# Optimization experiments

Hardware: AMD Instinct MI355X
Metric: run time of the kernel (lower is better)

The kernel has to match this reference:

```python
import jax, jax.numpy as jnp
import numpy as np

H, C = 4, 32          # num_heads, hidden_channels
NEG_ATT = 0.2         # GAT attention leaky_relu slope (PyG default)
NEG_ACT = 0.01        # F.leaky_relu default slope applied after each conv


def gat_conv(x_src, x_dst, Wsrc, Wdst, a_src, a_dst, bias, src_idx, dst_idx, n_dst):
    """One bipartite GATConv (add_self_loops=False, concat=True)."""
    hs = (x_src @ Wsrc).reshape(-1, H, C)            # [Ns,H,C]
    hd = (x_dst @ Wdst).reshape(-1, H, C)            # [Nd,H,C]
    a_s = (hs * a_src).sum(-1)                       # [Ns,H]
    a_d = (hd * a_dst).sum(-1)                       # [Nd,H]
    e = jax.nn.leaky_relu(a_s[src_idx] + a_d[dst_idx], NEG_ATT)  # [E,H]
    m = jax.ops.segment_max(e, dst_idx, num_segments=n_dst)      # [Nd,H]
    ex = jnp.exp(e - m[dst_idx])
    denom = jax.ops.segment_sum(ex, dst_idx, num_segments=n_dst)
    alpha = ex / (denom[dst_idx] + 1e-16)            # edge softmax over dst
    msg = hs[src_idx] * alpha[:, :, None]            # [E,H,C]
    out = jax.ops.segment_sum(msg, dst_idx, num_segments=n_dst)  # [Nd,H,C]
    return out.reshape(n_dst, H * C) + bias


def setup_inputs() -> dict:
    key = jax.random.key(0)
    ks = jax.random.split(key, 40)
    it = iter(range(40))
    Nu, Nm, E, D, O = 100000, 20000, 500000, 64, 64
    HC = H * C

    def rn(shape, s=0.1):
        return jax.random.normal(ks[next(it)], shape, jnp.float32) * s

    def ri(n, hi):
        return jax.random.randint(ks[next(it)], (n,), 0, hi)

    return {
        "user_ids": jnp.arange(Nu), "movie_ids": jnp.arange(Nm),
        "um_src": ri(E, Nu), "um_dst": ri(E, Nm),
        "mu_src": ri(E, Nm), "mu_dst": ri(E, Nu),
        "user_emb": rn((Nu, D)), "movie_emb": rn((Nm, D)),
        "l1_um_Wsrc": rn((D, HC)), "l1_um_Wdst": rn((D, HC)),
        "l1_um_asrc": rn((H, C)), "l1_um_adst": rn((H, C)), "l1_um_b": rn((HC,)),
        "l1_mu_Wsrc": rn((D, HC)), "l1_mu_Wdst": rn((D, HC)),
        "l1_mu_asrc": rn((H, C)), "l1_mu_adst": rn((H, C)), "l1_mu_b": rn((HC,)),
        "l2_um_W": rn((HC, HC)), "l2_um_asrc": rn((H, C)), "l2_um_adst": rn((H, C)), "l2_um_b": rn((HC,)),
        "l2_mu_W": rn((HC, HC)), "l2_mu_asrc": rn((H, C)), "l2_mu_adst": rn((H, C)), "l2_mu_b": rn((HC,)),
        "Wo": rn((HC, O)), "bo": rn((O,)),
    }


def reference(user_ids, movie_ids, um_src, um_dst, mu_src, mu_dst,
              user_emb, movie_emb,
              l1_um_Wsrc, l1_um_Wdst, l1_um_asrc, l1_um_adst, l1_um_b,
              l1_mu_Wsrc, l1_mu_Wdst, l1_mu_asrc, l1_mu_adst, l1_mu_b,
              l2_um_W, l2_um_asrc, l2_um_adst, l2_um_b,
              l2_mu_W, l2_mu_asrc, l2_mu_adst, l2_mu_b,
              Wo, bo):
    xu = user_emb[user_ids]
    xm = movie_emb[movie_ids]
    Nu, Nm = xu.shape[0], xm.shape[0]
    # layer 1 (HeteroConv sum: each dst type receives exactly one edge type here)
    hm = gat_conv(xu, xm, l1_um_Wsrc, l1_um_Wdst, l1_um_asrc, l1_um_adst, l1_um_b, um_src, um_dst, Nm)
    hu = gat_conv(xm, xu, l1_mu_Wsrc, l1_mu_Wdst, l1_mu_asrc, l1_mu_adst, l1_mu_b, mu_src, mu_dst, Nu)
    xu = jax.nn.leaky_relu(hu, NEG_ACT)
    xm = jax.nn.leaky_relu(hm, NEG_ACT)
    # layer 2 (non-bipartite in_channels int => shared lin for src and dst)
    hm = gat_conv(xu, xm, l2_um_W, l2_um_W, l2_um_asrc, l2_um_adst, l2_um_b, um_src, um_dst, Nm)
    hu = gat_conv(xm, xu, l2_mu_W, l2_mu_W, l2_mu_asrc, l2_mu_adst, l2_mu_b, mu_src, mu_dst, Nu)
    xu = jax.nn.leaky_relu(hu, NEG_ACT)
    xm = jax.nn.leaky_relu(hm, NEG_ACT)
    out_user = xu @ Wo + bo
    out_movie = xm @ Wo + bo
    return out_user, out_movie, xu, xm
```

## Files before the change

### kernel.cpp

```cpp
#include <hip/hip_runtime.h>
#include <hip/hip_bf16.h>
#include <cstdint>


#define HC 128
#define HH 4
#define WPART 256
#define EPB 2048

typedef __attribute__((ext_vector_type(8))) short bf16x8;
typedef __attribute__((ext_vector_type(4))) float f32x4;

__device__ __forceinline__ short f2bf(float f) {
    return __builtin_bit_cast(short, __float2bfloat16(f));
}
__device__ __forceinline__ float bf2f(ushort u) {
    return __builtin_bit_cast(float, ((unsigned)u) << 16);
}

struct VT { const float* W[8]; const float* a[8]; float* v[8]; };
__global__ void make_v_all_k(VT t) {
    int gid = blockIdx.x * 256 + threadIdx.x;
    int task, base;
    if (gid < 1024) { task = gid >> 8; base = gid & 255; }
    else if (gid < 3072) { int g = gid - 1024; task = 4 + (g >> 9); base = g & 511; }
    else return;
    int k = base >> 2, h = base & 3;
    int coff = (task & 1) * 4;
    const float* wr = t.W[task] + (size_t)k * HC + h * 32;
    const float* ar = t.a[task] + h * 32;
    float s = 0.f;
    #pragma unroll
    for (int c = 0; c < 32; ++c) s = fmaf(wr[c], ar[c], s);
    t.v[task][k * 8 + coff + h] = s;
}

struct PT { const float* W[5]; const float* V[5]; ushort* Wb[5];
            int K[5]; int Nw[5]; int start[6]; };
__global__ void pack_all_k(PT t) {
    int gid = blockIdx.x * 256 + threadIdx.x;
    if (gid >= t.start[5]) return;
    int task = 0;
    while (gid >= t.start[task + 1]) ++task;
    int loc = gid - t.start[task];
    int K = t.K[task], Nw = t.Nw[task];
    int n = loc / K, k = loc % K;
    float v = 0.f;
    if (n < Nw) v = t.W[task][(size_t)k * Nw + n];
    else if (t.V[task] != nullptr && n < Nw + 8) v = t.V[task][k * 8 + (n - Nw)];
    t.Wb[task][loc] = (ushort)f2bf(v);
}

template <int NT, int MODE, bool ABF>
__global__ __launch_bounds__(256) void gemm_dual_k(
    const void* A0, const int* idx0, const ushort* Wb0, ushort* hsb0,
    ushort* atts0, float* attd0, float* C0, const float* bias0, int M0, int nb0,
    const void* A1, const int* idx1, const ushort* Wb1, ushort* hsb1,
    ushort* atts1, float* attd1, float* C1, const float* bias1, int M1,
    int K, int ldc) {
    const void* A; const int* aidx; const ushort* Wb; ushort* hsb;
    ushort* atts; float* attd; float* C; const float* bias; int M, bid;
    if ((int)blockIdx.x < nb0) {
        A = A0; aidx = idx0; Wb = Wb0; hsb = hsb0; atts = atts0; attd = attd0;
        C = C0; bias = bias0; M = M0; bid = blockIdx.x;
    } else {
        A = A1; aidx = idx1; Wb = Wb1; hsb = hsb1; atts = atts1; attd = attd1;
        C = C1; bias = bias1; M = M1; bid = blockIdx.x - nb0;
    }
    int lane = threadIdx.x & 63;
    int wave = threadIdx.x >> 6;
    int m_base = bid * 128 + wave * 32;
    int lm = lane & 15;
    int kg = lane >> 4;

    int r0 = m_base + lm, r1 = r0 + 16;
    int cr0 = r0 < M ? r0 : M - 1;
    int cr1 = r1 < M ? r1 : M - 1;
    int row0 = aidx ? aidx[cr0] : cr0;
    int row1 = aidx ? aidx[cr1] : cr1;
    const ushort* bp = Wb + (size_t)lm * K + kg * 8;

    f32x4 acc[2][NT] = {};
    for (int k0 = 0; k0 < K; k0 += 32) {
        bf16x8 a[2];
        if (ABF) {
            const ushort* a0p = (const ushort*)A + (size_t)row0 * K + kg * 8;
            const ushort* a1p = (const ushort*)A + (size_t)row1 * K + kg * 8;
            a[0] = *reinterpret_cast<const bf16x8*>(a0p + k0);
            a[1] = *reinterpret_cast<const bf16x8*>(a1p + k0);
        } else {
            const float* a0p = (const float*)A + (size_t)row0 * K + kg * 8;
            const float* a1p = (const float*)A + (size_t)row1 * K + kg * 8;
            float af[2][8];
            *reinterpret_cast<float4*>(&af[0][0]) = *reinterpret_cast<const float4*>(a0p + k0);
            *reinterpret_cast<float4*>(&af[0][4]) = *reinterpret_cast<const float4*>(a0p + k0 + 4);
            *reinterpret_cast<float4*>(&af[1][0]) = *reinterpret_cast<const float4*>(a1p + k0);
            *reinterpret_cast<float4*>(&af[1][4]) = *reinterpret_cast<const float4*>(a1p + k0 + 4);
            #pragma unroll
            for (int mi = 0; mi < 2; ++mi)
                #pragma unroll
                for (int j = 0; j < 8; ++j) a[mi][j] = f2bf(af[mi][j]);
        }
        #pragma unroll
        for (int nt = 0; nt < NT; ++nt) {
            bf16x8 b = *reinterpret_cast<const bf16x8*>(bp + (size_t)nt * 16 * K + k0);
            acc[0][nt] = __builtin_amdgcn_mfma_f32_16x16x32_bf16(a[0], b, acc[0][nt], 0, 0, 0);
            acc[1][nt] = __builtin_amdgcn_mfma_f32_16x16x32_bf16(a[1], b, acc[1][nt], 0, 0, 0);
        }
    }
    #pragma unroll
    for (int mi = 0; mi < 2; ++mi) {
        int rowb = m_base + mi * 16 + kg * 4;
        if (MODE == 0) {
            #pragma unroll
            for (int nt = 0; nt < NT - 1; ++nt) {
                int col = nt * 16 + lm;
                #pragma unroll
                for (int r = 0; r < 4; ++r) {
                    int row = rowb + r;
                    if (row < M) hsb[(size_t)row * HC + col] = (ushort)f2bf(acc[mi][nt][r]);
                }
            }
            #pragma unroll
            for (int r = 0; r < 4; ++r) {
                int row = rowb + r;
                if (row < M) {
                    float v = acc[mi][NT - 1][r];
                    if (lm < 4) atts[(size_t)row * 4 + lm] = (ushort)f2bf(v);
                    else if (lm < 8) attd[(size_t)row * 4 + (lm - 4)] = v;
                }
            }
        } else {
            #pragma unroll
            for (int nt = 0; nt < NT; ++nt) {
                int col = nt * 16 + lm;
                float bv = bias[col];
                #pragma unroll
                for (int r = 0; r < 4; ++r) {
                    int row = rowb + r;
                    if (row < M) C[(size_t)row * ldc + col] = acc[mi][nt][r] + bv;
                }
            }
        }
    }
}

__global__ __launch_bounds__(256) void part_count_k(
    const int* __restrict__ d0, int E0,
    const int* __restrict__ d1, int E1, int Nm,
    int* __restrict__ cntmat, int NB1) {
    __shared__ int lh[WPART];
    int t = threadIdx.x;
    lh[t] = 0;
    __syncthreads();
    int base = blockIdx.x * EPB + t;
    #pragma unroll
    for (int j = 0; j < EPB / 256; ++j) {
        int e = base + j * 256;
        int key = -1;
        if (e < E0) key = d0[e];
        else if (e - E0 < E1) key = Nm + d1[e - E0];
        if (key >= 0) atomicAdd(&lh[key >> 9], 1);
    }
    __syncthreads();
    cntmat[(size_t)t * NB1 + blockIdx.x] = lh[t];
}

__global__ __launch_bounds__(256) void part_scatter_k(
    const int* __restrict__ s0, const int* __restrict__ d0, int E0,
    const int* __restrict__ s1, const int* __restrict__ d1, int E1, int Nm,
    const int* __restrict__ scanned, int NB1, int2* __restrict__ buf) {
    __shared__ int lb[WPART];
    __shared__ int lc[WPART];
    int t = threadIdx.x;
    lb[t] = scanned[(size_t)t * NB1 + blockIdx.x];
    lc[t] = 0;
    __syncthreads();
    int base = blockIdx.x * EPB + t;
    #pragma unroll
    for (int j = 0; j < EPB / 256; ++j) {
        int e = base + j * 256;
        int key = -1, src = 0;
        if (e < E0) { key = d0[e]; src = s0[e]; }
        else if (e - E0 < E1) { key = Nm + d1[e - E0]; src = s1[e - E0]; }
        if (key >= 0) {
            int w = key >> 9;
            int r = atomicAdd(&lc[w], 1);
            buf[lb[w] + r] = make_int2(src, key);
        }
    }
}

__global__ __launch_bounds__(512) void csort_k(
    const int2* __restrict__ buf, const int* __restrict__ scanned, int NB1,
    int E, int NK, int* __restrict__ rs, int* __restrict__ csr) {
    __shared__ int c1[512];
    __shared__ int ls[512];
    int b = blockIdx.x;
    int t = threadIdx.x;
    int lo = scanned[(size_t)b * NB1];
    int hi = (b + 1 < WPART) ? scanned[(size_t)(b + 1) * NB1] : E;
    int keylo = b << 9;
    c1[t] = 0;
    __syncthreads();
    for (int i = lo + t; i < hi; i += 512)
        atomicAdd(&c1[buf[i].y - keylo], 1);
    __syncthreads();
    int v = c1[t];
    ls[t] = v;
    __syncthreads();
    for (int off = 1; off < 512; off <<= 1) {
        int x = (t >= off) ? ls[t - off] : 0;
        __syncthreads();
        ls[t] += x;
        __syncthreads();
    }
    ls[t] -= v;
    int gk = keylo + t;
    if (gk <= NK) rs[gk] = lo + ls[t];
    c1[t] = 0;
    __syncthreads();
    for (int i = lo + t; i < hi; i += 512) {
        int2 p = buf[i];
        int k = p.y - keylo;
        int r = atomicAdd(&c1[k], 1);
        csr[lo + ls[k] + r] = p.x;
    }
}

__global__ void scan_block_k(const int* __restrict__ deg, int n,
                             int* __restrict__ out, int* __restrict__ partial) {
    __shared__ int s[256];
    int i = blockIdx.x * 256 + threadIdx.x;
    int v = (i < n) ? deg[i] : 0;
    s[threadIdx.x] = v;
    __syncthreads();
    for (int off = 1; off < 256; off <<= 1) {
        int x = (threadIdx.x >= off) ? s[threadIdx.x - off] : 0;
        __syncthreads();
        s[threadIdx.x] += x;
        __syncthreads();
    }
    if (i < n) out[i] = s[threadIdx.x] - v;
    if (threadIdx.x == 255) partial[blockIdx.x] = s[255];
}

__global__ void scan_partial_k(int* __restrict__ partial, int nb) {
    __shared__ int s[512];
    int t = threadIdx.x;
    int v = (t < nb) ? partial[t] : 0;
    s[t] = v;
    __syncthreads();
    for (int off = 1; off < 512; off <<= 1) {
        int x = (t >= off) ? s[t - off] : 0;
        __syncthreads();
        s[t] += x;
        __syncthreads();
    }
    if (t < nb) partial[t] = s[t] - v;
}

__global__ void add_off_k(int* __restrict__ out, const int* __restrict__ partial, int n) {
    int i = blockIdx.x * 256 + threadIdx.x;
    if (i < n) out[i] += partial[blockIdx.x];
}

template <bool WF32, bool WBF>
__global__ __launch_bounds__(256) void agg16_dual_k(
    const int* __restrict__ rs0, const int* __restrict__ csr0,
    const ushort* __restrict__ hsb0, const ushort* __restrict__ atts0,
    const float* __restrict__ attd0, const float* __restrict__ bias0,
    float* __restrict__ out0, ushort* __restrict__ outb0, int n0,
    const int* __restrict__ rs1, const int* __restrict__ csr1,
    const ushort* __restrict__ hsb1, const ushort* __restrict__ atts1,
    const float* __restrict__ attd1, const float* __restrict__ bias1,
    float* __restrict__ out1, ushort* __restrict__ outb1, int n1) {
    int g = (int)((blockIdx.x * 256u + threadIdx.x) >> 4);
    const int* rs; const int* csr; const ushort* hsb; const ushort* atts;
    const float* attd; const float* bias; float* out; ushort* outb; int node;
    if (g < n0) {
        rs = rs0; csr = csr0; hsb = hsb0; atts = atts0; attd = attd0;
        bias = bias0; out = out0; outb = outb0; node = g;
    } else {
        node = g - n0;
        if (node >= n1) return;
        rs = rs1; csr = csr1; hsb = hsb1; atts = atts1; attd = attd1;
        bias = bias1; out = out1; outb = outb1;
    }
    int c = threadIdx.x & 15;
    int h = c >> 2;
    float ad = attd[node * 4 + h];
    int s0 = rs[node], s1 = rs[node + 1];
    float acc[8] = {};
    float wsum = 0.f;
    int i = s0;
    for (; i + 4 <= s1; i += 4) {
        int sx[4];
        #pragma unroll
        for (int j = 0; j < 4; ++j) sx[j] = csr[i + j];
        bf16x8 hv[4]; float el[4];
        #pragma unroll
        for (int j = 0; j < 4; ++j) {
            hv[j] = *reinterpret_cast<const bf16x8*>(hsb + (size_t)sx[j] * HC + 8 * c);
            el[j] = bf2f(atts[(size_t)sx[j] * 4 + h]);
        }
        #pragma unroll
        for (int j = 0; j < 4; ++j) {
            float e = el[j] + ad;
            e = e > 0.f ? e : 0.2f * e;
            float w = __expf(e);
            wsum += w;
            #pragma unroll
            for (int k = 0; k < 8; ++k)
                acc[k] = fmaf(w, bf2f((ushort)hv[j][k]), acc[k]);
        }
    }
    for (; i < s1; ++i) {
        int src = csr[i];
        bf16x8 hv = *reinterpret_cast<const bf16x8*>(hsb + (size_t)src * HC + 8 * c);
        float e = bf2f(atts[(size_t)src * 4 + h]) + ad;
        e = e > 0.f ? e : 0.2f * e;
        float w = __expf(e);
        wsum += w;
        #pragma unroll
        for (int k = 0; k < 8; ++k)
            acc[k] = fmaf(w, bf2f((ushort)hv[k]), acc[k]);
    }
    float inv = 1.f / (wsum + 1e-16f);
    float v[8];
    #pragma unroll
    for (int k = 0; k < 8; ++k) {
        v[k] = fmaf(acc[k], inv, bias[8 * c + k]);
        v[k] = v[k] > 0.f ? v[k] : 0.01f * v[k];
    }
    if (WF32) {
        float4 o0 = make_float4(v[0], v[1], v[2], v[3]);
        float4 o1 = make_float4(v[4], v[5], v[6], v[7]);
        reinterpret_cast<float4*>(out + (size_t)node * HC + 8 * c)[0] = o0;
        reinterpret_cast<float4*>(out + (size_t)node * HC + 8 * c)[1] = o1;
    }
    if (WBF) {
        bf16x8 u;
        #pragma unroll
        for (int k = 0; k < 8; ++k) u[k] = f2bf(v[k]);
        *reinterpret_cast<bf16x8*>(outb + (size_t)node * HC + 8 * c) = u;
    }
}

extern "C" void kernel_launch(void* const* d_in, const int* in_sizes, int n_in,
                              void* d_out, int out_size, void* d_ws, size_t ws_size,
                              hipStream_t stream) {
    const int Nu = in_sizes[0];
    const int Nm = in_sizes[1];
    const int E1 = in_sizes[2];
    const int E2 = in_sizes[4];
    const int D  = in_sizes[6] / Nu;
    const int O  = in_sizes[27];
    const int E  = E1 + E2;
    const int NK = Nm + Nu;

    const int*   user_ids  = (const int*)d_in[0];
    const int*   movie_ids = (const int*)d_in[1];
    const int*   um_src    = (const int*)d_in[2];
    const int*   um_dst    = (const int*)d_in[3];
    const int*   mu_src    = (const int*)d_in[4];
    const int*   mu_dst    = (const int*)d_in[5];
    const float* user_emb  = (const float*)d_in[6];
    const float* movie_emb = (const float*)d_in[7];
    const float* l1_um_Wsrc = (const float*)d_in[8];
    const float* l1_um_Wdst = (const float*)d_in[9];
    const float* l1_um_asrc = (const float*)d_in[10];
    const float* l1_um_adst = (const float*)d_in[11];
    const float* l1_um_b    = (const float*)d_in[12];
    const float* l1_mu_Wsrc = (const float*)d_in[13];
    const float* l1_mu_Wdst = (const float*)d_in[14];
    const float* l1_mu_asrc = (const float*)d_in[15];
    const float* l1_mu_adst = (const float*)d_in[16];
    const float* l1_mu_b    = (const float*)d_in[17];
    const float* l2_um_W    = (const float*)d_in[18];
    const float* l2_um_asrc = (const float*)d_in[19];
    const float* l2_um_adst = (const float*)d_in[20];
    const float* l2_um_b    = (const float*)d_in[21];
    const float* l2_mu_W    = (const float*)d_in[22];
    const float* l2_mu_asrc = (const float*)d_in[23];
    const float* l2_mu_adst = (const float*)d_in[24];
    const float* l2_mu_b    = (const float*)d_in[25];
    const float* Wo         = (const float*)d_in[26];
    const float* bo         = (const float*)d_in[27];

    auto cdiv = [](int a, int b) { return (a + b - 1) / b; };
    const int NB1 = cdiv(E, EPB);
    const int CM  = WPART * NB1;

    char* p = (char*)d_ws;
    auto alloc = [&](size_t bytes) { void* r = p; p += (bytes + 255) & ~(size_t)255; return r; };
    ushort* hs_u = (ushort*)alloc((size_t)Nu * HC * 2);
    ushort* hs_m = (ushort*)alloc((size_t)Nm * HC * 2);
    ushort* XUb  = (ushort*)alloc((size_t)Nu * HC * 2);
    ushort* XMb  = (ushort*)alloc((size_t)Nm * HC * 2);
    ushort* atts_u = (ushort*)alloc((size_t)Nu * 4 * 2);
    ushort* atts_m = (ushort*)alloc((size_t)Nm * 4 * 2);
    float* attd_u = (float*)alloc((size_t)Nu * 4 * 4);
    float* attd_m = (float*)alloc((size_t)Nm * 4 * 4);
    float* V_u1  = (float*)alloc((size_t)HC * 8 * 4);
    float* V_m1  = (float*)alloc((size_t)HC * 8 * 4);
    float* V_u2  = (float*)alloc((size_t)HC * 8 * 4);
    float* V_m2  = (float*)alloc((size_t)HC * 8 * 4);
    ushort* Wb_u1 = (ushort*)alloc((size_t)144 * D * 2);
    ushort* Wb_m1 = (ushort*)alloc((size_t)144 * D * 2);
    ushort* Wb_u2 = (ushort*)alloc((size_t)144 * HC * 2);
    ushort* Wb_m2 = (ushort*)alloc((size_t)144 * HC * 2);
    ushort* Wb_o  = (ushort*)alloc((size_t)64 * HC * 2);
    int* rs      = (int*)alloc((size_t)(NK + 2) * 4);
    int* cntmat  = (int*)alloc((size_t)(CM + 256) * 4);
    int* scanned = (int*)alloc((size_t)(CM + 256) * 4);
    int2* buf    = (int2*)alloc((size_t)E * 8);
    int* csr     = (int*)alloc((size_t)E * 4);
    int* part    = (int*)alloc(1024 * 4);

    {
        VT vt;
        const float* Ws[8] = {l1_um_Wsrc, l1_mu_Wdst, l1_mu_Wsrc, l1_um_Wdst,
                              l2_um_W, l2_mu_W, l2_mu_W, l2_um_W};
        const float* as[8] = {l1_um_asrc, l1_mu_adst, l1_mu_asrc, l1_um_adst,
                              l2_um_asrc, l2_mu_adst, l2_mu_asrc, l2_um_adst};
        float* vs[8] = {V_u1, V_u1, V_m1, V_m1, V_u2, V_u2, V_m2, V_m2};
        for (int i = 0; i < 8; ++i) { vt.W[i] = Ws[i]; vt.a[i] = as[i]; vt.v[i] = vs[i]; }
        make_v_all_k<<<12, 256, 0, stream>>>(vt);

        PT pt;
        const float* pW[5] = {l1_um_Wsrc, l1_mu_Wsrc, l2_um_W, l2_mu_W, Wo};
        const float* pV[5] = {V_u1, V_m1, V_u2, V_m2, nullptr};
        ushort* pB[5] = {Wb_u1, Wb_m1, Wb_u2, Wb_m2, Wb_o};
        int pK[5] = {D, D, HC, HC, HC};
        int pN[5] = {HC, HC, HC, HC, 64};
        int cum = 0;
        for (int i = 0; i < 5; ++i) {
            pt.W[i] = pW[i]; pt.V[i] = pV[i]; pt.Wb[i] = pB[i];
            pt.K[i] = pK[i]; pt.Nw[i] = pN[i];
            pt.start[i] = cum;
            cum += (i < 4 ? 144 : 64) * pK[i];
        }
        pt.start[5] = cum;
        pack_all_k<<<cdiv(cum, 256), 256, 0, stream>>>(pt);
    }

    part_count_k<<<NB1, 256, 0, stream>>>(um_dst, E1, mu_dst, E2, Nm, cntmat, NB1);
    {
        int nb = cdiv(CM, 256);
        scan_block_k<<<nb, 256, 0, stream>>>(cntmat, CM, scanned, part);
        scan_partial_k<<<1, 512, 0, stream>>>(part, nb);
        add_off_k<<<nb, 256, 0, stream>>>(scanned, part, CM);
    }
    part_scatter_k<<<NB1, 256, 0, stream>>>(um_src, um_dst, E1, mu_src, mu_dst, E2,
                                            Nm, scanned, NB1, buf);
    csort_k<<<WPART, 512, 0, stream>>>(buf, scanned, NB1, E, NK, rs, csr);

    float* OU = (float*)d_out;
    float* OM = OU + (size_t)Nu * O;
    float* XU = OM + (size_t)Nm * O;
    float* XM = XU + (size_t)Nu * HC;

    int gbU = cdiv(Nu, 128), gbM = cdiv(Nm, 128);
    int aggBlocks = cdiv((Nm + Nu) * 16, 256);

    gemm_dual_k<9, 0, false><<<gbU + gbM, 256, 0, stream>>>(
        user_emb, user_ids, Wb_u1, hs_u, atts_u, attd_u, nullptr, nullptr, Nu, gbU,
        movie_emb, movie_ids, Wb_m1, hs_m, atts_m, attd_m, nullptr, nullptr, Nm,
        D, 0);
    agg16_dual_k<false, true><<<aggBlocks, 256, 0, stream>>>(
        rs, csr, hs_u, atts_u, attd_m, l1_um_b, nullptr, XMb, Nm,
        rs + Nm, csr, hs_m, atts_m, attd_u, l1_mu_b, nullptr, XUb, Nu);

    gemm_dual_k<9, 0, true><<<gbU + gbM, 256, 0, stream>>>(
        XUb, nullptr, Wb_u2, hs_u, atts_u, attd_u, nullptr, nullptr, Nu, gbU,
        XMb, nullptr, Wb_m2, hs_m, atts_m, attd_m, nullptr, nullptr, Nm,
        HC, 0);
    agg16_dual_k<true, false><<<aggBlocks, 256, 0, stream>>>(
        rs, csr, hs_u, atts_u, attd_m, l2_um_b, XM, nullptr, Nm,
        rs + Nm, csr, hs_m, atts_m, attd_u, l2_mu_b, XU, nullptr, Nu);

    gemm_dual_k<4, 1, false><<<gbU + gbM, 256, 0, stream>>>(
        XU, nullptr, Wb_o, nullptr, nullptr, nullptr, OU, bo, Nu, gbU,
        XM, nullptr, Wb_o, nullptr, nullptr, nullptr, OM, bo, Nm,
        HC, O);
}
```

Baseline: 213.6 us.

## Fuse output projection into layer-2 aggregation kernel via MFMA epilogue

The final Wo projection GEMM is folded into the layer-2 aggregation kernel. Each block stages its 16 aggregated node rows as bf16 in shared memory and runs a 16x16x32 bf16 MFMA against Wo to write the output rows directly. This removes one kernel launch and the re-read of the fp32 XU/XM activations. In exchange it adds a block-wide barrier and shared-memory traffic to the aggregation kernel, and the projection now uses bf16-rounded activations.

```diff
diff --git a/kernel.cpp b/kernel.cpp
--- a/kernel.cpp
+++ b/kernel.cpp
@@ -265,7 +265,7 @@
     if (i < n) out[i] += partial[blockIdx.x];
 }
 
-template <bool WF32, bool WBF>
+template <bool WF32, bool WBF, bool PROJ>
 __global__ __launch_bounds__(256) void agg16_dual_k(
     const int* __restrict__ rs0, const int* __restrict__ csr0,
     const ushort* __restrict__ hsb0, const ushort* __restrict__ atts0,
@@ -274,23 +274,28 @@
     const int* __restrict__ rs1, const int* __restrict__ csr1,
     const ushort* __restrict__ hsb1, const ushort* __restrict__ atts1,
     const float* __restrict__ attd1, const float* __restrict__ bias1,
-    float* __restrict__ out1, ushort* __restrict__ outb1, int n1) {
+    float* __restrict__ out1, ushort* __restrict__ outb1, int n1,
+    const ushort* __restrict__ Wbo, const float* __restrict__ bo,
+    float* __restrict__ pj0, float* __restrict__ pj1) {
     int g = (int)((blockIdx.x * 256u + threadIdx.x) >> 4);
+    int gl = (threadIdx.x >> 4) & 15;
     const int* rs; const int* csr; const ushort* hsb; const ushort* atts;
-    const float* attd; const float* bias; float* out; ushort* outb; int node;
+    const float* attd; const float* bias; float* out; ushort* outb;
+    int node; bool active = true;
     if (g < n0) {
         rs = rs0; csr = csr0; hsb = hsb0; atts = atts0; attd = attd0;
         bias = bias0; out = out0; outb = outb0; node = g;
     } else {
         node = g - n0;
-        if (node >= n1) return;
+        if (node >= n1) { active = false; node = 0; }
         rs = rs1; csr = csr1; hsb = hsb1; atts = atts1; attd = attd1;
         bias = bias1; out = out1; outb = outb1;
     }
     int c = threadIdx.x & 15;
     int h = c >> 2;
     float ad = attd[node * 4 + h];
-    int s0 = rs[node], s1 = rs[node + 1];
+    int s0 = 0, s1 = 0;
+    if (active) { s0 = rs[node]; s1 = rs[node + 1]; }
     float acc[8] = {};
     float wsum = 0.f;
     int i = s0;
@@ -333,17 +338,47 @@
         v[k] = fmaf(acc[k], inv, bias[8 * c + k]);
         v[k] = v[k] > 0.f ? v[k] : 0.01f * v[k];
     }
-    if (WF32) {
+    if (active && WF32) {
         float4 o0 = make_float4(v[0], v[1], v[2], v[3]);
         float4 o1 = make_float4(v[4], v[5], v[6], v[7]);
         reinterpret_cast<float4*>(out + (size_t)node * HC + 8 * c)[0] = o0;
         reinterpret_cast<float4*>(out + (size_t)node * HC + 8 * c)[1] = o1;
     }
-    if (WBF) {
+    if (active && WBF) {
         bf16x8 u;
         #pragma unroll
         for (int k = 0; k < 8; ++k) u[k] = f2bf(v[k]);
         *reinterpret_cast<bf16x8*>(outb + (size_t)node * HC + 8 * c) = u;
+    }
+    if constexpr (PROJ) {
+        __shared__ ushort As[16][136];
+        bf16x8 u;
+        #pragma unroll
+        for (int k = 0; k < 8; ++k) u[k] = active ? f2bf(v[k]) : (short)0;
+        *reinterpret_cast<bf16x8*>(&As[gl][8 * c]) = u;
+        __syncthreads();
+        int lane = threadIdx.x & 63;
+        int wv = threadIdx.x >> 6;
+        int lm = lane & 15;
+        int kg = lane >> 4;
+        int col = wv * 16 + lm;
+        const ushort* bp = Wbo + (size_t)col * HC + kg * 8;
+        f32x4 pacc = {};
+        #pragma unroll
+        for (int k0 = 0; k0 < HC; k0 += 32) {
+            bf16x8 a = *reinterpret_cast<const bf16x8*>(&As[lm][k0 + kg * 8]);
+            bf16x8 b = *reinterpret_cast<const bf16x8*>(bp + k0);
+            pacc = __builtin_amdgcn_mfma_f32_16x16x32_bf16(a, b, pacc, 0, 0, 0);
+        }
+        float bv = bo[col];
+        int blockBase = blockIdx.x * 16;
+        #pragma unroll
+        for (int r = 0; r < 4; ++r) {
+            int slot = kg * 4 + r;
+            int ng = blockBase + slot;
+            if (ng < n0) pj0[(size_t)ng * 64 + col] = pacc[r] + bv;
+            else if (ng - n0 < n1) pj1[(size_t)(ng - n0) * 64 + col] = pacc[r] + bv;
+        }
     }
 }
 
@@ -468,20 +503,17 @@
         user_emb, user_ids, Wb_u1, hs_u, atts_u, attd_u, nullptr, nullptr, Nu, gbU,
         movie_emb, movie_ids, Wb_m1, hs_m, atts_m, attd_m, nullptr, nullptr, Nm,
         D, 0);
-    agg16_dual_k<false, true><<<aggBlocks, 256, 0, stream>>>(
+    agg16_dual_k<false, true, false><<<aggBlocks, 256, 0, stream>>>(
         rs, csr, hs_u, atts_u, attd_m, l1_um_b, nullptr, XMb, Nm,
-        rs + Nm, csr, hs_m, atts_m, attd_u, l1_mu_b, nullptr, XUb, Nu);
+        rs + Nm, csr, hs_m, atts_m, attd_u, l1_mu_b, nullptr, XUb, Nu,
+        nullptr, nullptr, nullptr, nullptr);
 
     gemm_dual_k<9, 0, true><<<gbU + gbM, 256, 0, stream>>>(
         XUb, nullptr, Wb_u2, hs_u, atts_u, attd_u, nullptr, nullptr, Nu, gbU,
         XMb, nullptr, Wb_m2, hs_m, atts_m, attd_m, nullptr, nullptr, Nm,
         HC, 0);
-    agg16_dual_k<true, false><<<aggBlocks, 256, 0, stream>>>(
+    agg16_dual_k<true, false, true><<<aggBlocks, 256, 0, stream>>>(
         rs, csr, hs_u, atts_u, attd_m, l2_um_b, XM, nullptr, Nm,
-        rs + Nm, csr, hs_m, atts_m, attd_u, l2_mu_b, XU, nullptr, Nu);
-
-    gemm_dual_k<4, 1, false><<<gbU + gbM, 256, 0, stream>>>(
-        XU, nullptr, Wb_o, nullptr, nullptr, nullptr, OU, bo, Nu, gbU,
-        XM, nullptr, Wb_o, nullptr, nullptr, nullptr, OM, bo, Nm,
-        HC, O);
-}
+        rs + Nm, csr, hs_m, atts_m, attd_u, l2_mu_b, XU, nullptr, Nu,
+        Wb_o, bo, OM, OU);
+}
```

After: 209.0 us. 2.2% less time.
